# Optimization experiments

Measured on AMD Instinct MI355X. Metric: run time of the kernel, lower is better.

The kernel has to match this reference:

```python
import jax, jax.numpy as jnp
import numpy as np

B, S, H = 4, 2048, 4096   # batch, seq, hidden
Q_DIM = 32 * 128          # num_attention_heads * head_dim
KV_DIM = 8 * 128          # num_key_value_heads * head_dim
R = 16                    # lora_r
SCALING = 32.0 / 16.0     # lora_alpha / lora_r


def setup_inputs() -> dict:
    key = jax.random.key(0)
    ks = jax.random.split(key, 10)
    def n(k, shape, scale):
        return jax.random.normal(k, shape, dtype=jnp.float32) * scale
    x = jax.random.normal(ks[0], (B, S, H), dtype=jnp.float32)
    # base weights stored as [out_dim, in_dim] like nn.Linear
    Wq = n(ks[1], (Q_DIM, H), 0.02)
    Wk = n(ks[2], (KV_DIM, H), 0.02)
    Wv = n(ks[3], (KV_DIM, H), 0.02)
    bq = n(ks[4], (Q_DIM,), 0.02)
    bk = n(ks[5], (KV_DIM,), 0.02)
    bv = n(ks[6], (KV_DIM,), 0.02)
    # LoRA A: kaiming-uniform-like init; B: zeros in training start, use small
    # random values here so the LoRA path is numerically exercised.
    bound = 1.0 / np.sqrt(H)
    Aq = jax.random.uniform(ks[7], (H, R), jnp.float32, -bound, bound)
    Ak = jax.random.uniform(ks[8], (H, R), jnp.float32, -bound, bound)
    Av = jax.random.uniform(ks[9], (H, R), jnp.float32, -bound, bound)
    kb = jax.random.split(jax.random.fold_in(key, 1), 3)
    Bq = n(kb[0], (R, Q_DIM), 0.01)
    Bk = n(kb[1], (R, KV_DIM), 0.01)
    Bv = n(kb[2], (R, KV_DIM), 0.01)
    return {"x": x, "Wq": Wq, "Wk": Wk, "Wv": Wv, "bq": bq, "bk": bk, "bv": bv,
            "Aq": Aq, "Bq": Bq, "Ak": Ak, "Bk": Bk, "Av": Av, "Bv": Bv}


def _proj(x, W, b, A, Bm):
    # base GEMM + low-rank LoRA delta + bias (dropout p=0 -> identity)
    base = jnp.einsum('bsh,oh->bso', x, W)
    delta = jnp.einsum('bsr,ro->bso', jnp.einsum('bsh,hr->bsr', x, A), Bm)
    return base + SCALING * delta + b


def reference(x, Wq, Wk, Wv, bq, bk, bv, Aq, Bq, Ak, Bk, Av, Bv):
    q = _proj(x, Wq, bq, Aq, Bq)  # [B,S,Q_DIM]
    k = _proj(x, Wk, bk, Ak, Bk)  # [B,S,KV_DIM]
    v = _proj(x, Wv, bv, Av, Bv)  # [B,S,KV_DIM]
    return q, k, v
```

## Files before the change

kernel.cpp:

```cpp
#include <hip/hip_runtime.h>


#define GLOBAL_AS __attribute__((address_space(1)))
#define LDS_AS    __attribute__((address_space(3)))

typedef __attribute__((ext_vector_type(8))) short  short8;
typedef __attribute__((ext_vector_type(4))) float  floatx4;

constexpr int Mdim = 8192;
constexpr int Kdim = 4096;
constexpr int NQ   = 4096;
constexpr int NKV  = 1024;
constexpr int NTOT = NQ + 2 * NKV;
constexpr float LORA_SCALE = 2.0f;

constexpr int BM = 256, BN = 256;
constexpr int TILES_M = Mdim / BM;
constexpr int TILES_N = NTOT / BN;
constexpr int NWG = TILES_M * TILES_N;
constexpr int NSLICE = Kdim / 32;

constexpr int WEFF_BLOCKS = (NTOT / 64) * (Kdim / 512);
constexpr int CVT_BLOCKS  = 2048;
constexpr int AT_STRIDE   = 516;

__device__ __forceinline__ unsigned short f2bf(float f) {
    union { float f; unsigned int u; } a; a.f = f;
    unsigned int r = a.u + 0x7FFFu + ((a.u >> 16) & 1u);
    return (unsigned short)(r >> 16);
}

__global__ __launch_bounds__(256)
void prep_kernel(const float4* __restrict__ x4, unsigned short* __restrict__ Xbf,
                 const float* __restrict__ Wq, const float* __restrict__ Wk,
                 const float* __restrict__ Wv,
                 const float* __restrict__ Aq, const float* __restrict__ Bq,
                 const float* __restrict__ Ak, const float* __restrict__ Bk,
                 const float* __restrict__ Av, const float* __restrict__ Bv,
                 unsigned short* __restrict__ Wf) {
    __shared__ float AsT[16 * AT_STRIDE];
    __shared__ float Bsc[64 * 16];

    const int tid = threadIdx.x;

    if (blockIdx.x >= WEFF_BLOCKS) {
        int i = (blockIdx.x - WEFF_BLOCKS) * 256 + tid;
        const int stride = CVT_BLOCKS * 256;
        const int n4 = Mdim * Kdim / 4;
        ushort4* out = (ushort4*)Xbf;
        for (; i < n4; i += stride) {
            float4 v = x4[i];
            ushort4 u;
            u.x = f2bf(v.x); u.y = f2bf(v.y); u.z = f2bf(v.z); u.w = f2bf(v.w);
            out[i] = u;
        }
        return;
    }

    const int n0 = (blockIdx.x >> 3) * 64;
    const int h0 = (blockIdx.x & 7) * 512;

    const float* W; const float* A; const float* Bm; int O; int nn0;
    if (n0 < NQ)            { W = Wq; A = Aq; Bm = Bq; O = NQ;  nn0 = n0; }
    else if (n0 < NQ + NKV) { W = Wk; A = Ak; Bm = Bk; O = NKV; nn0 = n0 - NQ; }
    else                    { W = Wv; A = Av; Bm = Bv; O = NKV; nn0 = n0 - NQ - NKV; }

    {
        const float4* Af4 = (const float4*)(A) + h0 * 4;
        #pragma unroll
        for (int i = 0; i < 8; ++i) {
            const int f = i * 256 + tid;
            const float4 v = Af4[f];
            const int hl = f >> 2;
            const int r0 = (f & 3) * 4;
            AsT[(r0 + 0) * AT_STRIDE + hl] = v.x;
            AsT[(r0 + 1) * AT_STRIDE + hl] = v.y;
            AsT[(r0 + 2) * AT_STRIDE + hl] = v.z;
            AsT[(r0 + 3) * AT_STRIDE + hl] = v.w;
        }
    }
    {
        const int nl = tid & 63;
        const int rq = tid >> 6;
        #pragma unroll
        for (int j = 0; j < 4; ++j) {
            const int r = rq * 4 + j;
            Bsc[nl * 16 + r] = Bm[r * O + nn0 + nl] * LORA_SCALE;
        }
    }
    __syncthreads();

    const int wv_ = tid >> 6;
    const int lane = tid & 63;

    #pragma unroll
    for (int pass = 0; pass < 2; ++pass) {
        const int hl = pass * 256 + lane * 4;
        float4 areg[16];
        #pragma unroll
        for (int r = 0; r < 16; ++r)
            areg[r] = *(const float4*)(&AsT[r * AT_STRIDE + hl]);

        for (int i = 0; i < 16; ++i) {
            const int nl = wv_ * 16 + i;
            const float4 w4 = *(const float4*)(W + (size_t)(nn0 + nl) * Kdim + h0 + hl);
            const float4* b4 = (const float4*)(&Bsc[nl * 16]);
            float4 d = {0.f, 0.f, 0.f, 0.f};
            #pragma unroll
            for (int q = 0; q < 4; ++q) {
                const float4 b = b4[q];
                d.x += areg[q*4+0].x * b.x + areg[q*4+1].x * b.y + areg[q*4+2].x * b.z + areg[q*4+3].x * b.w;
                d.y += areg[q*4+0].y * b.x + areg[q*4+1].y * b.y + areg[q*4+2].y * b.z + areg[q*4+3].y * b.w;
                d.z += areg[q*4+0].z * b.x + areg[q*4+1].z * b.y + areg[q*4+2].z * b.z + areg[q*4+3].z * b.w;
                d.w += areg[q*4+0].w * b.x + areg[q*4+1].w * b.y + areg[q*4+2].w * b.z + areg[q*4+3].w * b.w;
            }
            ushort4 u;
            u.x = f2bf(w4.x + d.x); u.y = f2bf(w4.y + d.y);
            u.z = f2bf(w4.z + d.z); u.w = f2bf(w4.w + d.w);
            *(ushort4*)(Wf + (size_t)(n0 + nl) * Kdim + h0 + hl) = u;
        }
    }
}

__global__ __launch_bounds__(512, 2)
void gemm_qkv_kernel(const unsigned short* __restrict__ X,
                     const unsigned short* __restrict__ Wf,
                     const float* __restrict__ bq, const float* __restrict__ bk,
                     const float* __restrict__ bv,
                     float* __restrict__ out) {
    __shared__ __align__(16) unsigned short Abuf[4][8192];
    __shared__ __align__(16) unsigned short Bbuf[4][8192];

    const int tid  = threadIdx.x;
    const int lane = tid & 63;
    const int w    = tid >> 6;
    const int wr   = w >> 2;
    const int wc   = w & 3;

    int bid = blockIdx.x;
    bid = (bid & 7) * (NWG / 8) + (bid >> 3);
    const int row0 = (bid / TILES_N) * BM;
    const int col0 = (bid % TILES_N) * BN;

    const int swz    = (((lane >> 4) ^ ((lane >> 1) & 3)) << 4);
    const int aByte0 = (wr * 128 + (lane & 15)) * 64 + swz;
    const int bByte0 = (wc * 64  + (lane & 15)) * 64 + swz;

    const int srow = (w << 4) + (lane >> 2);
    const int kswz = (((lane & 3) ^ ((lane >> 3) & 3)) << 3);
    const unsigned short* pA0 = X  + (size_t)(row0 + srow) * Kdim + kswz;
    const unsigned short* pA1 = pA0 + (size_t)128 * Kdim;
    const unsigned short* pB0 = Wf + (size_t)(col0 + srow) * Kdim + kswz;
    const unsigned short* pB1 = pB0 + (size_t)128 * Kdim;

    floatx4 acc[8][4];
    #pragma unroll
    for (int i = 0; i < 8; ++i)
        #pragma unroll
        for (int j = 0; j < 4; ++j)
            acc[i][j] = (floatx4){0.f, 0.f, 0.f, 0.f};

    short8 bf[4];

#define STAGE(MATA, SS)                                                          \
    { const int ss_ = (SS); const int st_ = (SS) & 3;                            \
      if (MATA) {                                                                \
        __builtin_amdgcn_global_load_lds((const GLOBAL_AS void*)(pA0 + ss_ * 32),\
            (LDS_AS void*)(&Abuf[st_][w * 512]),        16, 0, 0);               \
        __builtin_amdgcn_global_load_lds((const GLOBAL_AS void*)(pA1 + ss_ * 32),\
            (LDS_AS void*)(&Abuf[st_][4096 + w * 512]), 16, 0, 0);               \
      } else {                                                                   \
        __builtin_amdgcn_global_load_lds((const GLOBAL_AS void*)(pB0 + ss_ * 32),\
            (LDS_AS void*)(&Bbuf[st_][w * 512]),        16, 0, 0);               \
        __builtin_amdgcn_global_load_lds((const GLOBAL_AS void*)(pB1 + ss_ * 32),\
            (LDS_AS void*)(&Bbuf[st_][4096 + w * 512]), 16, 0, 0);               \
      } }

#define DO_PHASE(G, MH, DOSTAGE, SMATA, SS, WAITMODE)                            \
    {                                                                            \
      const int slot_ = (G) & 3;                                                 \
      const char* abase_ = (const char*)Abuf + slot_ * 16384;                    \
      short8 af[4];                                                              \
      _Pragma("unroll")                                                          \
      for (int mf = 0; mf < 4; ++mf)                                             \
        af[mf] = *(const short8*)(abase_ + aByte0 + ((MH) * 4 + mf) * 1024);     \
      if ((MH) == 0) {                                                           \
        const char* bbase_ = (const char*)Bbuf + slot_ * 16384;                  \
        _Pragma("unroll")                                                        \
        for (int nf = 0; nf < 4; ++nf)                                           \
          bf[nf] = *(const short8*)(bbase_ + bByte0 + nf * 1024);                \
      }                                                                          \
      if (DOSTAGE) STAGE(SMATA, SS);                                             \
      __builtin_amdgcn_s_barrier();                                              \
      asm volatile("s_waitcnt lgkmcnt(0)");                                      \
      __builtin_amdgcn_s_setprio(1);                                             \
      _Pragma("unroll")                                                          \
      for (int mf = 0; mf < 4; ++mf)                                             \
        _Pragma("unroll")                                                        \
        for (int nf = 0; nf < 4; ++nf)                                           \
          acc[(MH) * 4 + mf][nf] = __builtin_amdgcn_mfma_f32_16x16x32_bf16(      \
              af[mf], bf[nf], acc[(MH) * 4 + mf][nf], 0, 0, 0);                  \
      __builtin_amdgcn_s_setprio(0);                                             \
      if ((WAITMODE) == 1) asm volatile("s_waitcnt vmcnt(8)" ::: "memory");      \
      if ((WAITMODE) == 2) asm volatile("s_waitcnt vmcnt(4)" ::: "memory");      \
      if ((WAITMODE) == 3) asm volatile("s_waitcnt vmcnt(0)" ::: "memory");      \
      __builtin_amdgcn_s_barrier();                                              \
    }

    STAGE(1, 0); STAGE(0, 0);
    STAGE(1, 1); STAGE(0, 1);
    STAGE(1, 2); STAGE(0, 2);
    asm volatile("s_waitcnt vmcnt(8)" ::: "memory");
    __builtin_amdgcn_s_barrier();

    for (int j = 0; j < NSLICE / 4 - 1; ++j) {
        const int g0 = j * 4;
        DO_PHASE(g0 + 0, 0, 1, 1, g0 + 3, 0);
        DO_PHASE(g0 + 0, 1, 1, 0, g0 + 3, 1);
        DO_PHASE(g0 + 1, 0, 1, 1, g0 + 4, 0);
        DO_PHASE(g0 + 1, 1, 1, 0, g0 + 4, 1);
        DO_PHASE(g0 + 2, 0, 1, 1, g0 + 5, 0);
        DO_PHASE(g0 + 2, 1, 1, 0, g0 + 5, 1);
        DO_PHASE(g0 + 3, 0, 1, 1, g0 + 6, 0);
        DO_PHASE(g0 + 3, 1, 1, 0, g0 + 6, 1);
    }
    DO_PHASE(124, 0, 1, 1, 127, 0);
    DO_PHASE(124, 1, 1, 0, 127, 1);
    DO_PHASE(125, 0, 0, 0, 0,   0);
    DO_PHASE(125, 1, 0, 0, 0,   2);
    DO_PHASE(126, 0, 0, 0, 0,   0);
    DO_PHASE(126, 1, 0, 0, 0,   3);
    DO_PHASE(127, 0, 0, 0, 0,   0);
    DO_PHASE(127, 1, 0, 0, 0,   0);

#undef DO_PHASE
#undef STAGE

    float* obase; int ldo; const float* bias; int cofs;
    if (col0 < NQ) {
        obase = out;                             ldo = NQ;  bias = bq; cofs = 0;
    } else if (col0 < NQ + NKV) {
        obase = out + (size_t)Mdim * NQ;         ldo = NKV; bias = bk; cofs = NQ;
    } else {
        obase = out + (size_t)Mdim * (NQ + NKV); ldo = NKV; bias = bv; cofs = NQ + NKV;
    }

    #pragma unroll
    for (int nf = 0; nf < 4; ++nf) {
        const int col = col0 + wc * 64 + nf * 16 + (lane & 15) - cofs;
        const float b = bias[col];
        #pragma unroll
        for (int mf = 0; mf < 8; ++mf) {
            #pragma unroll
            for (int r = 0; r < 4; ++r) {
                const int row = row0 + wr * 128 + mf * 16 + (lane >> 4) * 4 + r;
                __builtin_nontemporal_store(acc[mf][nf][r] + b,
                                            &obase[(size_t)row * ldo + col]);
            }
        }
    }
}

extern "C" void kernel_launch(void* const* d_in, const int* in_sizes, int n_in,
                              void* d_out, int out_size, void* d_ws, size_t ws_size,
                              hipStream_t stream) {
    const float* x  = (const float*)d_in[0];
    const float* Wq = (const float*)d_in[1];
    const float* Wk = (const float*)d_in[2];
    const float* Wv = (const float*)d_in[3];
    const float* bq = (const float*)d_in[4];
    const float* bk = (const float*)d_in[5];
    const float* bv = (const float*)d_in[6];
    const float* Aq = (const float*)d_in[7];
    const float* Bq = (const float*)d_in[8];
    const float* Ak = (const float*)d_in[9];
    const float* Bk = (const float*)d_in[10];
    const float* Av = (const float*)d_in[11];
    const float* Bv = (const float*)d_in[12];
    float* out = (float*)d_out;

    unsigned short* Xbf = (unsigned short*)d_ws;
    unsigned short* Wf  = Xbf + (size_t)Mdim * Kdim;

    prep_kernel<<<WEFF_BLOCKS + CVT_BLOCKS, 256, 0, stream>>>(
        (const float4*)x, Xbf, Wq, Wk, Wv, Aq, Bq, Ak, Bk, Av, Bv, Wf);

    gemm_qkv_kernel<<<NWG, 512, 0, stream>>>(Xbf, Wf, bq, bk, bv, out);
}
```

Before: 442.0 us.

## Double-buffer LDS fragment reads to overlap with MFMA across phases

Splits each phase into register-double-buffered A/B fragment reads so the next slice's LDS reads are issued before the current MFMA block runs. This removes the lgkmcnt(0) wait that sat directly before each MFMA group. The vmcnt thresholds are retuned to match the new ordering. The cost is more VGPRs for the second fragment set, which could lower occupancy or cause spills, and the synchronisation around slot reuse becomes more delicate.

```diff
diff --git a/kernel.cpp b/kernel.cpp
--- a/kernel.cpp
+++ b/kernel.cpp
@@ -160,7 +160,8 @@
         for (int j = 0; j < 4; ++j)
             acc[i][j] = (floatx4){0.f, 0.f, 0.f, 0.f};
 
-    short8 bf[4];
+    short8 afr[2][4];
+    short8 bfr[2][4];
 
 #define STAGE(MATA, SS)                                                          \
     { const int ss_ = (SS); const int st_ = (SS) & 3;                            \
@@ -176,64 +177,83 @@
             (LDS_AS void*)(&Bbuf[st_][4096 + w * 512]), 16, 0, 0);               \
       } }
 
-#define DO_PHASE(G, MH, DOSTAGE, SMATA, SS, WAITMODE)                            \
-    {                                                                            \
-      const int slot_ = (G) & 3;                                                 \
-      const char* abase_ = (const char*)Abuf + slot_ * 16384;                    \
-      short8 af[4];                                                              \
+#define READA(SET, SLOT, MH)                                                     \
+    { const char* ab_ = (const char*)Abuf + (SLOT) * 16384;                      \
       _Pragma("unroll")                                                          \
       for (int mf = 0; mf < 4; ++mf)                                             \
-        af[mf] = *(const short8*)(abase_ + aByte0 + ((MH) * 4 + mf) * 1024);     \
-      if ((MH) == 0) {                                                           \
-        const char* bbase_ = (const char*)Bbuf + slot_ * 16384;                  \
-        _Pragma("unroll")                                                        \
-        for (int nf = 0; nf < 4; ++nf)                                           \
-          bf[nf] = *(const short8*)(bbase_ + bByte0 + nf * 1024);                \
-      }                                                                          \
-      if (DOSTAGE) STAGE(SMATA, SS);                                             \
-      __builtin_amdgcn_s_barrier();                                              \
-      asm volatile("s_waitcnt lgkmcnt(0)");                                      \
-      __builtin_amdgcn_s_setprio(1);                                             \
+        afr[SET][mf] = *(const short8*)(ab_ + aByte0 + ((MH) * 4 + mf) * 1024); }
+
+#define READB(SET, SLOT)                                                         \
+    { const char* bb_ = (const char*)Bbuf + (SLOT) * 16384;                      \
+      _Pragma("unroll")                                                          \
+      for (int nf = 0; nf < 4; ++nf)                                             \
+        bfr[SET][nf] = *(const short8*)(bb_ + bByte0 + nf * 1024); }
+
+#define MFMA16(ASET, BSET, MH)                                                   \
+    { __builtin_amdgcn_s_setprio(1);                                             \
       _Pragma("unroll")                                                          \
       for (int mf = 0; mf < 4; ++mf)                                             \
         _Pragma("unroll")                                                        \
         for (int nf = 0; nf < 4; ++nf)                                           \
           acc[(MH) * 4 + mf][nf] = __builtin_amdgcn_mfma_f32_16x16x32_bf16(      \
-              af[mf], bf[nf], acc[(MH) * 4 + mf][nf], 0, 0, 0);                  \
-      __builtin_amdgcn_s_setprio(0);                                             \
-      if ((WAITMODE) == 1) asm volatile("s_waitcnt vmcnt(8)" ::: "memory");      \
-      if ((WAITMODE) == 2) asm volatile("s_waitcnt vmcnt(4)" ::: "memory");      \
-      if ((WAITMODE) == 3) asm volatile("s_waitcnt vmcnt(0)" ::: "memory");      \
+              afr[ASET][mf], bfr[BSET][nf], acc[(MH) * 4 + mf][nf], 0, 0, 0);    \
+      __builtin_amdgcn_s_setprio(0); }
+
+#define WAITV(WM)                                                                \
+    { if ((WM) == 1) asm volatile("s_waitcnt vmcnt(6)" ::: "memory");            \
+      if ((WM) == 2) asm volatile("s_waitcnt vmcnt(4)" ::: "memory");            \
+      if ((WM) == 3) asm volatile("s_waitcnt vmcnt(0)" ::: "memory"); }
+
+#define PH_EVEN(SLOT, BSET, DOSTAGE, SS, WM)                                     \
+    { READA(1, SLOT, 1);                                                         \
+      if (DOSTAGE) STAGE(1, SS);                                                 \
       __builtin_amdgcn_s_barrier();                                              \
-    }
+      MFMA16(0, BSET, 0);                                                        \
+      WAITV(WM);                                                                 \
+      __builtin_amdgcn_s_barrier(); }
+
+#define PH_ODD(NSLOT, BSET, NBSET, DOPRE, DOSTAGE, SS, WM)                       \
+    { if (DOPRE) { READA(0, NSLOT, 0); READB(NBSET, NSLOT); }                    \
+      if (DOSTAGE) STAGE(0, SS);                                                 \
+      __builtin_amdgcn_s_barrier();                                              \
+      MFMA16(1, BSET, 1);                                                        \
+      WAITV(WM);                                                                 \
+      __builtin_amdgcn_s_barrier(); }
 
     STAGE(1, 0); STAGE(0, 0);
     STAGE(1, 1); STAGE(0, 1);
     STAGE(1, 2); STAGE(0, 2);
     asm volatile("s_waitcnt vmcnt(8)" ::: "memory");
     __builtin_amdgcn_s_barrier();
+    READA(0, 0, 0);
+    READB(0, 0);
 
     for (int j = 0; j < NSLICE / 4 - 1; ++j) {
         const int g0 = j * 4;
-        DO_PHASE(g0 + 0, 0, 1, 1, g0 + 3, 0);
-        DO_PHASE(g0 + 0, 1, 1, 0, g0 + 3, 1);
-        DO_PHASE(g0 + 1, 0, 1, 1, g0 + 4, 0);
-        DO_PHASE(g0 + 1, 1, 1, 0, g0 + 4, 1);
-        DO_PHASE(g0 + 2, 0, 1, 1, g0 + 5, 0);
-        DO_PHASE(g0 + 2, 1, 1, 0, g0 + 5, 1);
-        DO_PHASE(g0 + 3, 0, 1, 1, g0 + 6, 0);
-        DO_PHASE(g0 + 3, 1, 1, 0, g0 + 6, 1);
-    }
-    DO_PHASE(124, 0, 1, 1, 127, 0);
-    DO_PHASE(124, 1, 1, 0, 127, 1);
-    DO_PHASE(125, 0, 0, 0, 0,   0);
-    DO_PHASE(125, 1, 0, 0, 0,   2);
-    DO_PHASE(126, 0, 0, 0, 0,   0);
-    DO_PHASE(126, 1, 0, 0, 0,   3);
-    DO_PHASE(127, 0, 0, 0, 0,   0);
-    DO_PHASE(127, 1, 0, 0, 0,   0);
-
-#undef DO_PHASE
+        PH_EVEN((g0 + 0) & 3,     0,            1,  g0 + 3, 1);
+        PH_ODD ((g0 + 1) & 3,     0,   1,   1, 1,  g0 + 3, 0);
+        PH_EVEN((g0 + 1) & 3,     1,            1,  g0 + 4, 1);
+        PH_ODD ((g0 + 2) & 3,     1,   0,   1, 1,  g0 + 4, 0);
+        PH_EVEN((g0 + 2) & 3,     0,            1,  g0 + 5, 1);
+        PH_ODD ((g0 + 3) & 3,     0,   1,   1, 1,  g0 + 5, 0);
+        PH_EVEN((g0 + 3) & 3,     1,            1,  g0 + 6, 1);
+        PH_ODD ((g0 + 4) & 3,     1,   0,   1, 1,  g0 + 6, 0);
+    }
+    PH_EVEN(0, 0,        1, 127, 1);
+    PH_ODD (1, 0, 1,  1, 1, 127, 0);
+    PH_EVEN(1, 1,        0, 0,   2);
+    PH_ODD (2, 1, 0,  1, 0, 0,   0);
+    PH_EVEN(2, 0,        0, 0,   3);
+    PH_ODD (3, 0, 1,  1, 0, 0,   0);
+    PH_EVEN(3, 1,        0, 0,   0);
+    PH_ODD (0, 1, 0,  0, 0, 0,   0);
+
+#undef PH_ODD
+#undef PH_EVEN
+#undef WAITV
+#undef MFMA16
+#undef READB
+#undef READA
 #undef STAGE
 
     float* obase; int ldo; const float* bias; int cofs;
```

Result: slower. 461.2 us (+4.3%).
